# Performance work log

Hardware: AMD Instinct MI355X
Metric: run time of the kernel (lower is better)

## Reference

```python
import math
import jax, jax.numpy as jnp
import numpy as np

N_HEADS = 16   # matches init_kwargs n_heads
C_SAMPLING = 1  # matches init_kwargs c_sampling


def setup_inputs() -> dict:
    rng = jax.random.key(0)
    ks = jax.random.split(rng, 8)
    L = S = 2048
    B = 8
    D = 1024
    sc = 0.02  # weight scale
    return {
        "query": jax.random.normal(ks[0], (L, B, D), jnp.float32),
        "key": jax.random.normal(ks[1], (S, B, D), jnp.float32),
        "value": jax.random.normal(ks[2], (S, B, D), jnp.float32),
        "Wq": jax.random.normal(ks[3], (D, D), jnp.float32) * sc,
        "bq": jnp.zeros((D,), jnp.float32),
        "Wk": jax.random.normal(ks[4], (D, D), jnp.float32) * sc,
        "bk": jnp.zeros((D,), jnp.float32),
        "Wv": jax.random.normal(ks[5], (D, D), jnp.float32) * sc,
        "bv": jnp.zeros((D,), jnp.float32),
        "Wo": jax.random.normal(ks[6], (D, D), jnp.float32) * sc,
        "bo": jnp.zeros((D,), jnp.float32),
    }


def _autocorr_forward(query, key, value, Wq, bq, Wk, bk, Wv, bv, Wo, bo):
    L, B, D = query.shape
    S = key.shape[0]
    H = N_HEADS
    E = D // H

    def proj(x, W, b):
        return x @ W.T + b

    def to_attn(x):  # (T,B,D) -> (B,H,E,T)
        T = x.shape[0]
        return x.reshape(T, B, H, E).transpose(1, 2, 3, 0)

    Q = to_attn(proj(query, Wq, bq))   # (B,H,E,L)
    K = to_attn(proj(key, Wk, bk))     # (B,H,E,S)
    V = to_attn(proj(value, Wv, bv))   # (B,H,E,S)

    # Align K/V length to L (static shapes: branch resolved at trace time)
    if L > S:
        pad = [(0, 0)] * 3 + [(0, L - S)]
        K = jnp.pad(K, pad)
        V = jnp.pad(V, pad)
    else:
        K = K[..., :L]
        V = V[..., :L]

    # Cross-correlation via FFT along time axis
    Qf = jnp.fft.rfft(Q, axis=-1)
    Kf = jnp.fft.rfft(K, axis=-1)
    corr = jnp.fft.irfft(Qf * jnp.conj(Kf), n=L, axis=-1)  # (B,H,E,L)

    # --- time_delay_agg ---
    topk = int(C_SAMPLING * math.log(L))
    mean_corr = corr.mean(axis=-2)                         # (B,H,L)
    scores, taus = jax.lax.top_k(mean_corr, topk)          # (B,H,topk)
    w = jax.nn.softmax(scores, axis=-1)                    # (B,H,topk)
    # delayed index (s + tau) mod L : (B,H,L,topk)
    idx = (jnp.arange(L)[None, None, :, None] + taus[:, :, None, :]) % L
    # gather V along time: (B,H,E,L,topk)
    delayed = jnp.take_along_axis(V[:, :, :, :, None], idx[:, :, None, :, :], axis=3)
    agg = jnp.mean(delayed * w[:, :, None, None, :], axis=-1)  # (B,H,E,L)

    # recover_from_attn: (B,H,E,L) -> (L,B,H*E)
    out = agg.transpose(3, 0, 1, 2).reshape(L, B, H * E)
    return out @ Wo.T + bo  # (L,B,D); need_weights=False so corr is dropped


def reference(query, key, value, Wq, bq, Wk, bk, Wv, bv, Wo, bo):
    return _autocorr_forward(query, key, value, Wq, bq, Wk, bk, Wv, bv, Wo, bo)
```

## Files before the change

kernel.cpp:

```cpp
#include <hip/hip_runtime.h>
#include <math.h>

#define TOPK 7

typedef __attribute__((ext_vector_type(8))) short bf16x8;
typedef __attribute__((ext_vector_type(4))) float f32x4;

__device__ __forceinline__ void glds16(const ushort* g, ushort* l)
{
    __builtin_amdgcn_global_load_lds(
        (const __attribute__((address_space(1))) void*)g,
        (__attribute__((address_space(3))) void*)l, 16, 0, 0);
}

__device__ __forceinline__ void split1(float x, ushort& h, ushort& lo)
{
    union U { float f; unsigned u; };
    U a; a.f = x;
    unsigned r = (a.u + 0x7FFFu + ((a.u >> 16) & 1u)) >> 16;
    h = (ushort)r;
    U b; b.u = r << 16;
    U d; d.f = x - b.f;
    unsigned r2 = (d.u + 0x7FFFu + ((d.u >> 16) & 1u)) >> 16;
    lo = (ushort)r2;
}

__global__ __launch_bounds__(256)
void split_f32(const float* __restrict__ x, ushort* __restrict__ hi,
               ushort* __restrict__ lo, int n4)
{
    for (int i = blockIdx.x * 256 + threadIdx.x; i < n4; i += gridDim.x * 256) {
        float4 v = ((const float4*)x)[i];
        ushort4 h, lw;
        split1(v.x, h.x, lw.x);
        split1(v.y, h.y, lw.y);
        split1(v.z, h.z, lw.z);
        split1(v.w, h.w, lw.w);
        ((ushort4*)hi)[i] = h;
        ((ushort4*)lo)[i] = lw;
    }
}

__global__ __launch_bounds__(512, 2)
void gemm_split(const ushort* __restrict__ Ah, const ushort* __restrict__ Al,
                const ushort* __restrict__ Bh, const ushort* __restrict__ Bl,
                const float* __restrict__ bias, float* __restrict__ C)
{
    __shared__ ushort lds[65536];
    const int tid = threadIdx.x;
    const int w = tid >> 6, l = tid & 63;

    const int ord = blockIdx.y * gridDim.x + blockIdx.x;
    const int cpx = (gridDim.x * gridDim.y) >> 3;
    const int swz = (ord & 7) * cpx + (ord >> 3);
    const int bx = swz & 3;
    const int by = swz >> 2;

    const int wm = w >> 2, wn = w & 3;
    const int lr = l & 15, kgr = l >> 4;

    const ushort* gbB[4]; size_t goB[4]; int loB[4];
    const ushort* gbA[4]; size_t goA[4]; int loA[4];
#pragma unroll
    for (int q = 0; q < 4; ++q) {
        int idx = w * 4 + q;
        int cb = idx >> 4;
        int kg = (idx >> 2) & 3;
        int rblk = idx & 3;
        gbB[q] = cb ? Bl : Bh;
        goB[q] = (size_t)(bx * 256 + rblk * 64 + l) * 1024 + kg * 8;
        loB[q] = 16384 + cb * 8192 + kg * 2048 + rblk * 512;
        gbA[q] = cb ? Al : Ah;
        goA[q] = (size_t)(by * 256 + rblk * 64 + l) * 1024 + kg * 8;
        loA[q] = cb * 8192 + kg * 2048 + rblk * 512;
    }

    f32x4 acc[8][4];
#pragma unroll
    for (int i = 0; i < 8; ++i)
#pragma unroll
        for (int j = 0; j < 4; ++j) acc[i][j] = (f32x4){0.f, 0.f, 0.f, 0.f};

#define STAGE_B(bufbase_, k0_) do { \
    const int _bb = (bufbase_); const int _kk = (k0_); \
    _Pragma("unroll") \
    for (int q = 0; q < 4; ++q) \
        glds16(gbB[q] + goB[q] + _kk, &lds[_bb + loB[q]]); \
} while (0)

#define STAGE_A2(bufbase_, k0_, qa_, qb_) do { \
    const int _bb = (bufbase_); const int _kk = (k0_); \
    glds16(gbA[qa_] + goA[qa_] + _kk, &lds[_bb + loA[qa_]]); \
    glds16(gbA[qb_] + goA[qb_] + _kk, &lds[_bb + loA[qb_]]); \
} while (0)

#define COMPUTE2(i0_) do { \
    _Pragma("unroll") \
    for (int ii = 0; ii < 2; ++ii) { \
        const int i = (i0_) + ii; \
        const int ra = wm * 128 + i * 16 + lr; \
        bf16x8 fah = *(const bf16x8*)&lb[       kgr * 2048 + ra * 8]; \
        bf16x8 fal = *(const bf16x8*)&lb[8192 + kgr * 2048 + ra * 8]; \
        __builtin_amdgcn_s_setprio(1); \
        _Pragma("unroll") \
        for (int j = 0; j < 4; ++j) \
            acc[i][j] = __builtin_amdgcn_mfma_f32_16x16x32_bf16(fah, fbh[j], acc[i][j], 0, 0, 0); \
        _Pragma("unroll") \
        for (int j = 0; j < 4; ++j) \
            acc[i][j] = __builtin_amdgcn_mfma_f32_16x16x32_bf16(fah, fbl[j], acc[i][j], 0, 0, 0); \
        _Pragma("unroll") \
        for (int j = 0; j < 4; ++j) \
            acc[i][j] = __builtin_amdgcn_mfma_f32_16x16x32_bf16(fal, fbh[j], acc[i][j], 0, 0, 0); \
        __builtin_amdgcn_s_setprio(0); \
    } \
} while (0)

    STAGE_B(0, 0);       STAGE_A2(0, 0, 0, 1);       STAGE_A2(0, 0, 2, 3);
    STAGE_B(32768, 32);  STAGE_A2(32768, 32, 0, 1);  STAGE_A2(32768, 32, 2, 3);
    asm volatile("s_waitcnt vmcnt(8)" ::: "memory");
    __builtin_amdgcn_s_barrier();

#pragma unroll 2
    for (int t = 0; t < 32; ++t) {
        const int cb = (t & 1) * 32768;
        const ushort* lb = &lds[cb];
        const bool pre = (t < 30);
        const int kn = (t + 2) * 32;

        bf16x8 fbh[4], fbl[4];
#pragma unroll
        for (int j = 0; j < 4; ++j) {
            int rb = wn * 64 + j * 16 + lr;
            fbh[j] = *(const bf16x8*)&lb[16384 + kgr * 2048 + rb * 8];
            fbl[j] = *(const bf16x8*)&lb[24576 + kgr * 2048 + rb * 8];
        }
        COMPUTE2(0);
        __builtin_amdgcn_s_barrier();

        if (pre) STAGE_B(cb, kn);
        COMPUTE2(2);
        __builtin_amdgcn_s_barrier();

        if (pre) STAGE_A2(cb, kn, 0, 2);
        COMPUTE2(4);
        __builtin_amdgcn_s_barrier();

        COMPUTE2(6);
        __builtin_amdgcn_s_barrier();
        if (pre) {
            STAGE_A2(cb, kn, 1, 3);
            asm volatile("s_waitcnt vmcnt(8)" ::: "memory");
        } else {
            asm volatile("s_waitcnt vmcnt(0)" ::: "memory");
        }
        __builtin_amdgcn_s_barrier();
    }
#undef STAGE_B
#undef STAGE_A2
#undef COMPUTE2

#pragma unroll
    for (int j = 0; j < 4; ++j) {
        int col = bx * 256 + wn * 64 + j * 16 + lr;
        float bb = bias[col];
#pragma unroll
        for (int i = 0; i < 8; ++i) {
            int row0 = by * 256 + wm * 128 + i * 16 + kgr * 4;
#pragma unroll
            for (int reg = 0; reg < 4; ++reg)
                C[(size_t)(row0 + reg) * 1024 + col] = acc[i][j][reg] + bb;
        }
    }
}

__global__ __launch_bounds__(256)
void transpose_bhet(const float* __restrict__ src, float* __restrict__ dst)
{
    __shared__ float tile[64][129];
    const int tid = threadIdx.x;
    const int bh = blockIdx.x;
    const int b = bh >> 4, h = bh & 15;
    const int t0 = blockIdx.y * 128;
    const float* sp = src + (size_t)(t0 * 8 + b) * 1024 + h * 64;
#pragma unroll
    for (int i = 0; i < 8; ++i) {
        int idx = i * 256 + tid;
        int t = idx >> 4;
        int e4 = (idx & 15) * 4;
        float4 v = *(const float4*)(sp + (size_t)t * 8192 + e4);
        tile[e4 + 0][t] = v.x; tile[e4 + 1][t] = v.y; tile[e4 + 2][t] = v.z; tile[e4 + 3][t] = v.w;
    }
    __syncthreads();
    float* dp = dst + (size_t)bh * 64 * 2048 + t0;
#pragma unroll
    for (int i = 0; i < 8; ++i) {
        int idx = i * 256 + tid;
        int e = idx >> 5;
        int t4 = (idx & 31) * 4;
        float4 o;
        o.x = tile[e][t4]; o.y = tile[e][t4 + 1]; o.z = tile[e][t4 + 2]; o.w = tile[e][t4 + 3];
        *(float4*)(dp + (size_t)e * 2048 + t4) = o;
    }
}

__device__ __forceinline__ float2 cadd(float2 a, float2 b){ return make_float2(a.x+b.x, a.y+b.y); }
__device__ __forceinline__ float2 csub(float2 a, float2 b){ return make_float2(a.x-b.x, a.y-b.y); }
__device__ __forceinline__ float2 cmul(float2 a, float2 b){ return make_float2(a.x*b.x - a.y*b.y, a.x*b.y + a.y*b.x); }

__global__ __launch_bounds__(256)
void corr_fwd(const float* __restrict__ Qa, const float* __restrict__ Ka,
              float2* __restrict__ Spart)
{
    __shared__ float2 za[2048];
    __shared__ float2 zb[2048];
    __shared__ float2 tw[1024];
    const int tid = threadIdx.x;
    const int bh = blockIdx.x;
    const int eg = blockIdx.y;

#pragma unroll
    for (int r = 0; r < 4; ++r) {
        int u = tid + 256 * r;
        float sn, cs;
        sincospif((float)u * (1.0f / 1024.0f), &sn, &cs);
        tw[u] = make_float2(cs, -sn);
    }

    float2 sacc[4];
#pragma unroll
    for (int r = 0; r < 4; ++r) sacc[r] = make_float2(0.f, 0.f);
    float2 sacc1024 = make_float2(0.f, 0.f);

    const float* q0 = Qa + ((size_t)bh * 64 + eg * 8) * 2048;
    const float* k0 = Ka + ((size_t)bh * 64 + eg * 8) * 2048;

    for (int e = 0; e < 8; ++e) {
        const float* qr = q0 + (size_t)e * 2048;
        const float* kr = k0 + (size_t)e * 2048;
        for (int t = tid; t < 2048; t += 256)
            za[t] = make_float2(qr[t], kr[t]);
        __syncthreads();
        float2* x = za; float2* y = zb;
#pragma unroll 1
        for (int st = 0; st < 11; ++st) {
            const int s = 1 << st;
#pragma unroll
            for (int ui = 0; ui < 4; ++ui) {
                int u = ui * 256 + tid;
                int q = u & (s - 1);
                int ps = u - q;
                float2 a  = x[u];
                float2 bb = x[u + 1024];
                float2 wv = tw[ps];
                int i1 = 2 * ps + q;
                y[i1]     = cadd(a, bb);
                y[i1 + s] = cmul(csub(a, bb), wv);
            }
            __syncthreads();
            float2* tsw = x; x = y; y = tsw;
        }
#pragma unroll
        for (int r = 0; r < 4; ++r) {
            int f = tid + 256 * r;
            float2 A  = x[f];
            float2 Bc = x[(2048 - f) & 2047];
            float Ur = A.x + Bc.x, Ui = A.y - Bc.y;
            float Vr = A.x - Bc.x, Vi = -A.y - Bc.y;
            sacc[r].x += 0.25f * (-(Ur * Vi + Ui * Vr));
            sacc[r].y += 0.25f * ( Ur * Vr - Ui * Vi );
        }
        if (tid == 0) {
            float2 A = x[1024];
            float Ur = 2.f * A.x;
            float Vi = -2.f * A.y;
            sacc1024.x += 0.25f * (-(Ur * Vi));
            sacc1024.y += 0.25f * 0.f;
        }
        __syncthreads();
    }
    float2* sp = Spart + ((size_t)bh * 8 + eg) * 1025;
#pragma unroll
    for (int r = 0; r < 4; ++r) sp[tid + 256 * r] = sacc[r];
    if (tid == 0) sp[1024] = sacc1024;
}

__global__ __launch_bounds__(256)
void corr_inv_topk(const float2* __restrict__ Spart,
                   int* __restrict__ taus, float* __restrict__ wout)
{
    __shared__ float2 za[2048];
    __shared__ float2 zb[2048];
    __shared__ float2 tw[1024];
    __shared__ float2 Sh[1025];
    __shared__ float  redv[256];
    __shared__ int    redi[256];
    __shared__ float  sc[TOPK];
    __shared__ int    si[TOPK];

    const int tid = threadIdx.x;
    const int bh = blockIdx.x;

#pragma unroll
    for (int r = 0; r < 4; ++r) {
        int u = tid + 256 * r;
        float sn, cs;
        sincospif((float)u * (1.0f / 1024.0f), &sn, &cs);
        tw[u] = make_float2(cs, -sn);
    }

    const float2* sp0 = Spart + (size_t)bh * 8 * 1025;
    for (int f = tid; f < 1025; f += 256) {
        float2 s = make_float2(0.f, 0.f);
#pragma unroll
        for (int g = 0; g < 8; ++g) {
            float2 v = sp0[(size_t)g * 1025 + f];
            s.x += v.x; s.y += v.y;
        }
        Sh[f] = s;
    }
    __syncthreads();
    for (int f = tid; f < 2048; f += 256) {
        float2 v = (f <= 1024) ? make_float2(Sh[f].x, -Sh[f].y) : Sh[2048 - f];
        za[f] = v;
    }
    __syncthreads();
    float2* xi = za; float2* yi = zb;
#pragma unroll 1
    for (int st = 0; st < 11; ++st) {
        const int s = 1 << st;
#pragma unroll
        for (int ui = 0; ui < 4; ++ui) {
            int u = ui * 256 + tid;
            int q = u & (s - 1);
            int ps = u - q;
            float2 a  = xi[u];
            float2 bb = xi[u + 1024];
            float2 wv = tw[ps];
            int i1 = 2 * ps + q;
            yi[i1]     = cadd(a, bb);
            yi[i1 + s] = cmul(csub(a, bb), wv);
        }
        __syncthreads();
        float2* tsw = xi; xi = yi; yi = tsw;
    }

    for (int k = 0; k < TOPK; ++k) {
        float bvv = -INFINITY; int bii = 0;
        for (int t = tid; t < 2048; t += 256) {
            float v = xi[t].x;
            if (v > bvv) { bvv = v; bii = t; }
        }
        redv[tid] = bvv; redi[tid] = bii;
        __syncthreads();
        for (int off = 128; off > 0; off >>= 1) {
            if (tid < off) {
                float ov = redv[tid + off]; int oi = redi[tid + off];
                if (ov > redv[tid] || (ov == redv[tid] && oi < redi[tid])) { redv[tid] = ov; redi[tid] = oi; }
            }
            __syncthreads();
        }
        if (tid == 0) { sc[k] = redv[0]; si[k] = redi[0]; xi[redi[0]].x = -INFINITY; }
        __syncthreads();
    }
    if (tid == 0) {
        const float scale = 1.0f / (2048.0f * 64.0f);
        float m = sc[0] * scale;
        float ex[TOPK]; float ssum = 0.f;
        for (int k = 0; k < TOPK; ++k) { ex[k] = expf(sc[k] * scale - m); ssum += ex[k]; }
        for (int k = 0; k < TOPK; ++k) {
            taus[bh * TOPK + k] = si[k];
            wout[bh * TOPK + k] = ex[k] / ssum;
        }
    }
}

__global__ __launch_bounds__(256)
void agg_gather(const float* __restrict__ Vp, const int* __restrict__ taus,
                const float* __restrict__ w, ushort* __restrict__ ah,
                ushort* __restrict__ al)
{
    const int tid = threadIdx.x;
    const int bh = blockIdx.x;
    const int b = bh >> 4, h = bh & 15;
    const int t0 = blockIdx.y * 256;
    __shared__ int   stau[TOPK];
    __shared__ float sw[TOPK];
    if (tid < TOPK) { stau[tid] = taus[bh * TOPK + tid]; sw[tid] = w[bh * TOPK + tid] * (1.0f / TOPK); }
    __syncthreads();
    const float* vb = Vp + (size_t)b * 1024 + h * 64;
    ushort* ahb = ah + (size_t)b * 1024 + h * 64;
    ushort* alb = al + (size_t)b * 1024 + h * 64;
#pragma unroll
    for (int i = 0; i < 16; ++i) {
        int idx = i * 256 + tid;
        int t  = t0 + (idx >> 4);
        int e4 = (idx & 15) * 4;
        float a0 = 0.f, a1 = 0.f, a2 = 0.f, a3 = 0.f;
#pragma unroll
        for (int k = 0; k < TOPK; ++k) {
            int ts = (t + stau[k]) & 2047;
            float4 v = *(const float4*)(vb + (size_t)ts * 8192 + e4);
            a0 = fmaf(sw[k], v.x, a0); a1 = fmaf(sw[k], v.y, a1);
            a2 = fmaf(sw[k], v.z, a2); a3 = fmaf(sw[k], v.w, a3);
        }
        ushort4 hh, ll;
        split1(a0, hh.x, ll.x); split1(a1, hh.y, ll.y);
        split1(a2, hh.z, ll.z); split1(a3, hh.w, ll.w);
        *(ushort4*)(ahb + (size_t)t * 8192 + e4) = hh;
        *(ushort4*)(alb + (size_t)t * 8192 + e4) = ll;
    }
}

extern "C" void kernel_launch(void* const* d_in, const int* in_sizes, int n_in,
                              void* d_out, int out_size, void* d_ws, size_t ws_size,
                              hipStream_t stream)
{
    (void)in_sizes; (void)n_in; (void)out_size;
    const float* query = (const float*)d_in[0];
    const float* key   = (const float*)d_in[1];
    const float* value = (const float*)d_in[2];
    const float* Wq = (const float*)d_in[3];
    const float* bq = (const float*)d_in[4];
    const float* Wk = (const float*)d_in[5];
    const float* bk = (const float*)d_in[6];
    const float* Wv = (const float*)d_in[7];
    const float* bv = (const float*)d_in[8];
    const float* Wo = (const float*)d_in[9];
    const float* bo = (const float*)d_in[10];
    float* out = (float*)d_out;

    const size_t NEL  = (size_t)16777216;
    const size_t HEL  = NEL / 2;
    const size_t WEL  = (size_t)1048576;
    const size_t SLOTB = (size_t)64 * 1024 * 1024;

    char* ws = (char*)d_ws;
    float*  s1 = (float*)ws;
    char*   s2 = ws + SLOTB;
    char*   s3 = ws + 2 * SLOTB;
    int*    dtaus = (int*)(ws + 3 * SLOTB);
    float*  dw    = (float*)(dtaus + 128 * TOPK);
    const bool big_ws = ws_size >= 3 * SLOTB + (size_t)16 * 1024 * 1024;

    dim3 blk(256);
    dim3 gblk(512);
    dim3 gemm_full(4, 64), gemm_half(4, 32);
    dim3 tr_grid(128, 16);

    split_f32<<<1024, blk, 0, stream>>>(Wq, (ushort*)s3, (ushort*)s3 + WEL, (int)(WEL / 4));
    split_f32<<<2048, blk, 0, stream>>>(query, (ushort*)s2, (ushort*)s2 + NEL, (int)(NEL / 4));
    gemm_split<<<gemm_full, gblk, 0, stream>>>((ushort*)s2, (ushort*)s2 + NEL,
                                               (ushort*)s3, (ushort*)s3 + WEL, bq, s1);
    transpose_bhet<<<tr_grid, blk, 0, stream>>>(s1, (float*)s2);
    ushort* wkh = (ushort*)d_out;
    split_f32<<<1024, blk, 0, stream>>>(Wk, wkh, wkh + WEL, (int)(WEL / 4));
    split_f32<<<2048, blk, 0, stream>>>(key, (ushort*)s3, (ushort*)s3 + NEL, (int)(NEL / 4));
    gemm_split<<<gemm_full, gblk, 0, stream>>>((ushort*)s3, (ushort*)s3 + NEL,
                                               wkh, wkh + WEL, bk, s1);
    transpose_bhet<<<tr_grid, blk, 0, stream>>>(s1, (float*)s3);

    if (big_ws) {
        ushort* wvh = (ushort*)(ws + 3 * SLOTB + (size_t)8 * 1024 * 1024);
        split_f32<<<1024, blk, 0, stream>>>(Wv, wvh, wvh + WEL, (int)(WEL / 4));
        ushort* vsp = (ushort*)d_out;
        split_f32<<<2048, blk, 0, stream>>>(value, vsp, vsp + NEL, (int)(NEL / 4));
        gemm_split<<<gemm_full, gblk, 0, stream>>>(vsp, vsp + NEL, wvh, wvh + WEL,
                                                   bv, s1);
    } else {
        ushort* wvh = (ushort*)((char*)d_out + (size_t)32 * 1024 * 1024);
        split_f32<<<1024, blk, 0, stream>>>(Wv, wvh, wvh + WEL, (int)(WEL / 4));
        ushort* vsp = (ushort*)d_out;
        for (int hhalf = 0; hhalf < 2; ++hhalf) {
            split_f32<<<2048, blk, 0, stream>>>(value + hhalf * HEL, vsp, vsp + HEL, (int)(HEL / 4));
            gemm_split<<<gemm_half, gblk, 0, stream>>>(vsp, vsp + HEL, wvh, wvh + WEL,
                                                       bv, s1 + hhalf * HEL);
        }
    }

    float2* Spart = (float2*)d_out;
    corr_fwd<<<dim3(128, 8), blk, 0, stream>>>((const float*)s2, (const float*)s3, Spart);
    corr_inv_topk<<<dim3(128), blk, 0, stream>>>(Spart, dtaus, dw);
    agg_gather<<<dim3(128, 8), blk, 0, stream>>>(s1, dtaus, dw,
                                                 (ushort*)s2, (ushort*)s2 + NEL);
    split_f32<<<1024, blk, 0, stream>>>(Wo, (ushort*)s3, (ushort*)s3 + WEL, (int)(WEL / 4));
    gemm_split<<<gemm_full, gblk, 0, stream>>>((ushort*)s2, (ushort*)s2 + NEL,
                                               (ushort*)s3, (ushort*)s3 + WEL, bo, out);
}
```

Measured before the change: 691.3 us.

## Replace radix-2 Stockham FFT with radix-4 stages and XOR-swizzled LDS indexing

Both FFT kernels now call a shared 2048-point routine that runs five radix-4 Stockham stages plus one radix-2 stage instead of eleven radix-2 stages. This cuts the number of LDS passes and barriers and reduces twiddle multiplies. All LDS accesses go through an XOR swizzle meant to lessen bank conflicts on strided accesses. It adds some index arithmetic and register pressure, and the FFT is only one part of a pipeline that also contains large GEMMs.

```diff
diff --git a/kernel.cpp b/kernel.cpp
--- a/kernel.cpp
+++ b/kernel.cpp
@@ -52,9 +52,9 @@
 
     const int ord = blockIdx.y * gridDim.x + blockIdx.x;
     const int cpx = (gridDim.x * gridDim.y) >> 3;
-    const int swz = (ord & 7) * cpx + (ord >> 3);
-    const int bx = swz & 3;
-    const int by = swz >> 2;
+    const int swzb = (ord & 7) * cpx + (ord >> 3);
+    const int bx = swzb & 3;
+    const int by = swzb >> 2;
 
     const int wm = w >> 2, wn = w & 3;
     const int lr = l & 15, kgr = l >> 4;
@@ -207,6 +207,46 @@
 __device__ __forceinline__ float2 csub(float2 a, float2 b){ return make_float2(a.x-b.x, a.y-b.y); }
 __device__ __forceinline__ float2 cmul(float2 a, float2 b){ return make_float2(a.x*b.x - a.y*b.y, a.x*b.y + a.y*b.x); }
 
+__device__ __forceinline__ int swz(int i) { return i ^ ((i >> 4) & 15); }
+
+__device__ float2* fft2048(float2* x, float2* y, const float2* tw, int tid)
+{
+#pragma unroll 1
+    for (int st = 0; st < 5; ++st) {
+        const int s = 1 << (2 * st);
+#pragma unroll
+        for (int ui = 0; ui < 2; ++ui) {
+            const int u = ui * 256 + tid;
+            const int q = u & (s - 1);
+            const int ps = u - q;
+            float2 a = x[swz(u)],        b = x[swz(u + 512)];
+            float2 c = x[swz(u + 1024)], d = x[swz(u + 1536)];
+            float2 t0 = cadd(a, c), t1 = csub(a, c);
+            float2 t2 = cadd(b, d), tb = csub(b, d);
+            float2 t3 = make_float2(tb.y, -tb.x);
+            float2 w1 = tw[ps];
+            float2 w2 = tw[2 * ps];
+            float2 w3 = cmul(w1, w2);
+            const int o = 4 * ps + q;
+            y[swz(o)]         = cadd(t0, t2);
+            y[swz(o + s)]     = cmul(cadd(t1, t3), w1);
+            y[swz(o + 2 * s)] = cmul(csub(t0, t2), w2);
+            y[swz(o + 3 * s)] = cmul(csub(t1, t3), w3);
+        }
+        __syncthreads();
+        float2* tsw = x; x = y; y = tsw;
+    }
+#pragma unroll
+    for (int ui = 0; ui < 4; ++ui) {
+        const int u = ui * 256 + tid;
+        float2 a = x[swz(u)], b = x[swz(u + 1024)];
+        y[swz(u)]        = cadd(a, b);
+        y[swz(u + 1024)] = csub(a, b);
+    }
+    __syncthreads();
+    return y;
+}
+
 __global__ __launch_bounds__(256)
 void corr_fwd(const float* __restrict__ Qa, const float* __restrict__ Ka,
               float2* __restrict__ Spart)
@@ -238,39 +278,23 @@
         const float* qr = q0 + (size_t)e * 2048;
         const float* kr = k0 + (size_t)e * 2048;
         for (int t = tid; t < 2048; t += 256)
-            za[t] = make_float2(qr[t], kr[t]);
+            za[swz(t)] = make_float2(qr[t], kr[t]);
         __syncthreads();
-        float2* x = za; float2* y = zb;
-#pragma unroll 1
-        for (int st = 0; st < 11; ++st) {
-            const int s = 1 << st;
-#pragma unroll
-            for (int ui = 0; ui < 4; ++ui) {
-                int u = ui * 256 + tid;
-                int q = u & (s - 1);
-                int ps = u - q;
-                float2 a  = x[u];
-                float2 bb = x[u + 1024];
-                float2 wv = tw[ps];
-                int i1 = 2 * ps + q;
-                y[i1]     = cadd(a, bb);
-                y[i1 + s] = cmul(csub(a, bb), wv);
-            }
-            __syncthreads();
-            float2* tsw = x; x = y; y = tsw;
-        }
+
+        float2* res = fft2048(za, zb, tw, tid);
+
 #pragma unroll
         for (int r = 0; r < 4; ++r) {
             int f = tid + 256 * r;
-            float2 A  = x[f];
-            float2 Bc = x[(2048 - f) & 2047];
+            float2 A  = res[swz(f)];
+            float2 Bc = res[swz((2048 - f) & 2047)];
             float Ur = A.x + Bc.x, Ui = A.y - Bc.y;
             float Vr = A.x - Bc.x, Vi = -A.y - Bc.y;
             sacc[r].x += 0.25f * (-(Ur * Vi + Ui * Vr));
             sacc[r].y += 0.25f * ( Ur * Vr - Ui * Vi );
         }
         if (tid == 0) {
-            float2 A = x[1024];
+            float2 A = res[swz(1024)];
             float Ur = 2.f * A.x;
             float Vi = -2.f * A.y;
             sacc1024.x += 0.25f * (-(Ur * Vi));
@@ -321,33 +345,16 @@
     __syncthreads();
     for (int f = tid; f < 2048; f += 256) {
         float2 v = (f <= 1024) ? make_float2(Sh[f].x, -Sh[f].y) : Sh[2048 - f];
-        za[f] = v;
+        za[swz(f)] = v;
     }
     __syncthreads();
-    float2* xi = za; float2* yi = zb;
-#pragma unroll 1
-    for (int st = 0; st < 11; ++st) {
-        const int s = 1 << st;
-#pragma unroll
-        for (int ui = 0; ui < 4; ++ui) {
-            int u = ui * 256 + tid;
-            int q = u & (s - 1);
-            int ps = u - q;
-            float2 a  = xi[u];
-            float2 bb = xi[u + 1024];
-            float2 wv = tw[ps];
-            int i1 = 2 * ps + q;
-            yi[i1]     = cadd(a, bb);
-            yi[i1 + s] = cmul(csub(a, bb), wv);
-        }
-        __syncthreads();
-        float2* tsw = xi; xi = yi; yi = tsw;
-    }
+
+    float2* res = fft2048(za, zb, tw, tid);
 
     for (int k = 0; k < TOPK; ++k) {
         float bvv = -INFINITY; int bii = 0;
         for (int t = tid; t < 2048; t += 256) {
-            float v = xi[t].x;
+            float v = res[swz(t)].x;
             if (v > bvv) { bvv = v; bii = t; }
         }
         redv[tid] = bvv; redi[tid] = bii;
@@ -359,7 +366,7 @@
             }
             __syncthreads();
         }
-        if (tid == 0) { sc[k] = redv[0]; si[k] = redi[0]; xi[redi[0]].x = -INFINITY; }
+        if (tid == 0) { sc[k] = redv[0]; si[k] = redi[0]; res[swz(redi[0])].x = -INFINITY; }
         __syncthreads();
     }
     if (tid == 0) {
```

Result: faster. 626.1 us (-9.4%).
